# Performance work log

Measured on AMD Instinct MI355X. Metric: run time of the kernel, lower is better.

The kernel has to match this reference:

```python
import jax, jax.numpy as jnp
import numpy as np

EMB = 768
HEADS = 12
HEAD_DIM = EMB // HEADS


def setup_inputs() -> dict:
    key = jax.random.key(0)
    ks = jax.random.split(key, 9)
    B, L, D = 4, 2048, EMB
    s = 1.0 / np.sqrt(D)
    return {
        "x": jax.random.normal(ks[0], (B, L, D), dtype=jnp.float32),
        "Wq": jax.random.normal(ks[1], (D, D), dtype=jnp.float32) * s,
        "bq": jnp.zeros((D,), dtype=jnp.float32),
        "Wk": jax.random.normal(ks[2], (D, D), dtype=jnp.float32) * s,
        "bk": jnp.zeros((D,), dtype=jnp.float32),
        "Wv": jax.random.normal(ks[3], (D, D), dtype=jnp.float32) * s,
        "bv": jnp.zeros((D,), dtype=jnp.float32),
        "Wo": jax.random.normal(ks[4], (D, D), dtype=jnp.float32) * s,
        "bo": jnp.zeros((D,), dtype=jnp.float32),
    }


def reference(x, Wq, bq, Wk, bk, Wv, bv, Wo, bo):
    B, L, D = x.shape
    H, hd = HEADS, HEAD_DIM
    # QKV projections -> [B, H, L, hd]
    def proj(W, b):
        return (x @ W + b).reshape(B, L, H, hd).transpose(0, 2, 1, 3)
    Q = proj(Wq, bq)
    K = proj(Wk, bk)
    V = proj(Wv, bv)
    # scores [B, H, L, L]
    scores = jnp.einsum("bhqd,bhkd->bhqk", Q, K) / jnp.sqrt(jnp.float32(hd))
    attn = jax.nn.softmax(scores, axis=-1)
    out = jnp.einsum("bhqk,bhkd->bhqd", attn, V)  # [B,H,L,hd]
    out = out.transpose(0, 2, 1, 3).reshape(B, L, D)
    return out @ Wo + bo
```

## Files before the change

### kernel.cpp

```cpp
#include <hip/hip_runtime.h>
#include <math.h>

#define TL 2048
#define TD 768
#define NH 12
#define HD 64
#define NB 4
#define MTOT (NB * TL)

typedef __bf16 bf16;
typedef __attribute__((ext_vector_type(4))) __bf16 bf16x4;
typedef __attribute__((ext_vector_type(8))) __bf16 bf16x8;
typedef __attribute__((ext_vector_type(4))) float floatx4;

#define QSCALE 0.18033688011112042f

#define MFMA16(A, B, C) __builtin_amdgcn_mfma_f32_16x16x32_bf16(A, B, C, 0, 0, 0)

__device__ __forceinline__ void gl_lds16(const void* g, void* l) {
    __builtin_amdgcn_global_load_lds(
        (const __attribute__((address_space(1))) void*)g,
        (__attribute__((address_space(3))) void*)l, 16, 0, 0);
}

__device__ __forceinline__ floatx4 exp2x4(floatx4 a) {
    floatx4 r;
    r.x = __builtin_amdgcn_exp2f(a.x);
    r.y = __builtin_amdgcn_exp2f(a.y);
    r.z = __builtin_amdgcn_exp2f(a.z);
    r.w = __builtin_amdgcn_exp2f(a.w);
    return r;
}

__device__ __forceinline__ int kperm_inv(int r) {
    return (r & 35) | (((r >> 2) & 3) << 3) | (((r >> 4) & 1) << 2);
}

__global__ __launch_bounds__(256)
void prep_kernel(const float* __restrict__ x, bf16* __restrict__ xb,
                 const float* __restrict__ W0, const float* __restrict__ W1,
                 const float* __restrict__ W2, const float* __restrict__ W3,
                 bf16* __restrict__ T0, bf16* __restrict__ T1,
                 bf16* __restrict__ T2, bf16* __restrict__ T3)
{
    __shared__ float Ts[64][65];
    const int t = threadIdx.x;

    if (blockIdx.x < 6144) {
        size_t i = ((size_t)blockIdx.x * 256 + t) * 4;
        float4 v = *(const float4*)(x + i);
        bf16x4 o;
        o[0] = (bf16)v.x; o[1] = (bf16)v.y; o[2] = (bf16)v.z; o[3] = (bf16)v.w;
        *(bf16x4*)(xb + i) = o;
        return;
    }

    const int bid = blockIdx.x - 6144;
    const int z = bid / 144, rem = bid % 144;
    const float* W = z == 0 ? W0 : z == 1 ? W1 : z == 2 ? W2 : W3;
    bf16*       T = z == 0 ? T0 : z == 1 ? T1 : z == 2 ? T2 : T3;
    const int k0 = (rem % 12) * 64, n0 = (rem / 12) * 64;
    const int rr = t >> 4, cc = (t & 15) * 4;
#pragma unroll
    for (int i = 0; i < 4; ++i) {
        int row = rr + i * 16;
        float4 v = *(const float4*)(W + (size_t)(k0 + row) * TD + n0 + cc);
        Ts[row][cc] = v.x; Ts[row][cc + 1] = v.y;
        Ts[row][cc + 2] = v.z; Ts[row][cc + 3] = v.w;
    }
    __syncthreads();
#pragma unroll
    for (int i = 0; i < 4; ++i) {
        int n = rr + i * 16;
        bf16x4 pk;
#pragma unroll
        for (int j = 0; j < 4; ++j) pk[j] = (bf16)Ts[cc + j][n];
        *(bf16x4*)(T + (size_t)(n0 + n) * TD + k0 + cc) = pk;
    }
}

__global__ __launch_bounds__(256)
void qkv_gemm(const bf16* __restrict__ xb,
              const bf16* __restrict__ Wqt, const bf16* __restrict__ Wkt,
              const bf16* __restrict__ Wvt,
              const float* __restrict__ bq, const float* __restrict__ bk,
              const float* __restrict__ bv,
              bf16* __restrict__ Q, bf16* __restrict__ K, bf16* __restrict__ Vt)
{
    __shared__ __align__(16) bf16 SM[2 * 128 * 64];
    bf16* As = SM;
    bf16* Bs = SM + 128 * 64;

    const int t = threadIdx.x;
    const int lane = t & 63, w = t >> 6;
    const int quad = lane >> 4, l16 = lane & 15;
    const int m0 = blockIdx.x * 128;
    const int n0 = blockIdx.y * 128;
    const int which = blockIdx.z;
    const bf16*  W    = which == 0 ? Wqt : which == 1 ? Wkt : Wvt;
    const float* bias = which == 0 ? bq  : which == 1 ? bk  : bv;
    const float scale = which == 0 ? QSCALE : 1.0f;

    const int rm = (w >> 1) * 64, cn = (w & 1) * 64;

    floatx4 acc[4][4];
#pragma unroll
    for (int i = 0; i < 4; ++i)
#pragma unroll
        for (int j = 0; j < 4; ++j) acc[i][j] = (floatx4){0.f, 0.f, 0.f, 0.f};

    const bf16* gA[4];
    const bf16* gB[4];
#pragma unroll
    for (int i = 0; i < 4; ++i) {
        int n = t + i * 256, r = n >> 3, s = ((n & 7) ^ (r & 7)) * 8;
        gA[i] = xb + (size_t)(m0 + r) * TD + s;
        gB[i] = W + (size_t)(n0 + r) * TD + s;
    }

    for (int kk = 0; kk < TD; kk += 64) {
#pragma unroll
        for (int i = 0; i < 4; ++i) {
            gl_lds16(gA[i] + kk, As + t * 8 + i * 2048);
            gl_lds16(gB[i] + kk, Bs + t * 8 + i * 2048);
        }
        __syncthreads();
#pragma unroll
        for (int ks = 0; ks < 2; ++ks) {
            bf16x8 af[4], bfr[4];
#pragma unroll
            for (int mb = 0; mb < 4; ++mb) {
                int r = rm + mb * 16 + l16;
                af[mb] = *(const bf16x8*)&As[r * 64 + (((ks * 4 + quad) ^ (r & 7)) * 8)];
            }
#pragma unroll
            for (int nb = 0; nb < 4; ++nb) {
                int r = cn + nb * 16 + l16;
                bfr[nb] = *(const bf16x8*)&Bs[r * 64 + (((ks * 4 + quad) ^ (r & 7)) * 8)];
            }
#pragma unroll
            for (int mb = 0; mb < 4; ++mb)
#pragma unroll
                for (int nb = 0; nb < 4; ++nb)
                    acc[mb][nb] = MFMA16(af[mb], bfr[nb], acc[mb][nb]);
        }
        __syncthreads();
    }

    float bsc[4];
#pragma unroll
    for (int nb = 0; nb < 4; ++nb)
        bsc[nb] = bias[n0 + cn + nb * 16 + l16] * scale;

    const int token0 = m0 + rm;
    const int b  = token0 >> 11;
    const int l0 = token0 & (TL - 1);
    const int h  = (n0 + cn) >> 6;
    const int bh = b * NH + h;
    bf16* Ew = SM + w * (16 * 72);

    if (which < 2) {
        bf16* gp = (which == 0 ? Q : K) + ((size_t)bh * TL + l0) * HD;
#pragma unroll
        for (int mb = 0; mb < 4; ++mb) {
#pragma unroll
            for (int nb = 0; nb < 4; ++nb)
#pragma unroll
                for (int r = 0; r < 4; ++r)
                    Ew[(quad * 4 + r) * 72 + nb * 16 + l16] =
                        (bf16)(acc[mb][nb][r] * scale + bsc[nb]);
#pragma unroll
            for (int i = 0; i < 2; ++i) {
                int row = i * 8 + (lane >> 3), seg = lane & 7;
                bf16x8 v = *(const bf16x8*)&Ew[row * 72 + seg * 8];
                *(bf16x8*)(gp + (size_t)(mb * 16 + row) * HD + seg * 8) = v;
            }
        }
    } else {
#pragma unroll
        for (int nb = 0; nb < 4; ++nb) {
#pragma unroll
            for (int mb = 0; mb < 4; ++mb) {
                bf16x4 pk;
#pragma unroll
                for (int r = 0; r < 4; ++r) pk[r] = (bf16)(acc[mb][nb][r] + bsc[nb]);
                *(bf16x4*)&Ew[l16 * 72 + mb * 16 + quad * 4] = pk;
            }
#pragma unroll
            for (int i = 0; i < 2; ++i) {
                int row = i * 8 + (lane >> 3), seg = lane & 7;
                bf16x8 v = *(const bf16x8*)&Ew[row * 72 + seg * 8];
                *(bf16x8*)(Vt + ((size_t)bh * HD + nb * 16 + row) * TL + l0 + seg * 8) = v;
            }
        }
    }
}

__global__ __launch_bounds__(256)
void attn_kernel(const bf16* __restrict__ Q, const bf16* __restrict__ K,
                 const bf16* __restrict__ Vt, bf16* __restrict__ O)
{
    __shared__ __align__(16) bf16 Ks[64 * 64];
    __shared__ __align__(16) bf16 Vs[64 * 64];

    const int t = threadIdx.x;
    const int lane = t & 63, w = t >> 6;
    const int quad = lane >> 4, l16 = lane & 15;

    const int n = blockIdx.y * gridDim.x + blockIdx.x;
    const int xcd = n & 7, s = n >> 3;
    const int bh = xcd * 6 + (s >> 4);
    const int q0 = (s & 15) * 128;

    const bf16* Qb = Q + (size_t)bh * TL * HD;
    const bf16* Kb = K + (size_t)bh * TL * HD;
    const bf16* Vb = Vt + (size_t)bh * HD * TL;

    const int qw = q0 + w * 32;
    bf16x8 qf[2][2];
#pragma unroll
    for (int mb = 0; mb < 2; ++mb)
#pragma unroll
        for (int ks = 0; ks < 2; ++ks)
            qf[mb][ks] = *(const bf16x8*)(Qb + (size_t)(qw + mb * 16 + l16) * HD
                                          + ks * 32 + quad * 8);

    float lrow[2] = {0.f, 0.f};
    floatx4 o[2][4];
#pragma unroll
    for (int mb = 0; mb < 2; ++mb)
#pragma unroll
        for (int db = 0; db < 4; ++db) o[mb][db] = (floatx4){0.f, 0.f, 0.f, 0.f};

    const bf16* gK[2];
    const bf16* gV[2];
#pragma unroll
    for (int i = 0; i < 2; ++i) {
        int nn = t + i * 256, r = nn >> 3, sg = ((nn & 7) ^ (r & 7)) * 8;
        gK[i] = Kb + (size_t)kperm_inv(r) * HD + sg;
        gV[i] = Vb + (size_t)r * TL + sg;
    }

    for (int kt = 0; kt < TL / 64; ++kt) {
        const int k0 = kt * 64;
        __syncthreads();
#pragma unroll
        for (int i = 0; i < 2; ++i) {
            gl_lds16(gK[i] + (size_t)k0 * HD, Ks + t * 8 + i * 2048);
            gl_lds16(gV[i] + k0,              Vs + t * 8 + i * 2048);
        }
        __syncthreads();

        floatx4 s2[2][4];
#pragma unroll
        for (int nb = 0; nb < 4; ++nb) {
            int r = nb * 16 + l16;
            bf16x8 kf0 = *(const bf16x8*)&Ks[r * 64 + ((quad ^ (r & 7)) * 8)];
            bf16x8 kf1 = *(const bf16x8*)&Ks[r * 64 + (((4 + quad) ^ (r & 7)) * 8)];
#pragma unroll
            for (int mb = 0; mb < 2; ++mb) {
                floatx4 a = (floatx4){0.f, 0.f, 0.f, 0.f};
                a = MFMA16(kf0, qf[mb][0], a);
                a = MFMA16(kf1, qf[mb][1], a);
                s2[mb][nb] = a;
            }
        }

        bf16x8 pA[2][2];
#pragma unroll
        for (int mb = 0; mb < 2; ++mb) {
#pragma unroll
            for (int ks = 0; ks < 2; ++ks) {
                floatx4 p0 = exp2x4(s2[mb][2 * ks]);
                floatx4 p1 = exp2x4(s2[mb][2 * ks + 1]);
                lrow[mb] += (p0.x + p0.y + p0.z + p0.w) + (p1.x + p1.y + p1.z + p1.w);
                bf16x8 pk;
                pk[0] = (bf16)p0.x; pk[1] = (bf16)p0.y; pk[2] = (bf16)p0.z; pk[3] = (bf16)p0.w;
                pk[4] = (bf16)p1.x; pk[5] = (bf16)p1.y; pk[6] = (bf16)p1.z; pk[7] = (bf16)p1.w;
                pA[mb][ks] = pk;
            }
        }

#pragma unroll
        for (int ks = 0; ks < 2; ++ks) {
#pragma unroll
            for (int db = 0; db < 4; ++db) {
                int r = db * 16 + l16;
                bf16x8 vf = *(const bf16x8*)&Vs[r * 64 + (((ks * 4 + quad) ^ (r & 7)) * 8)];
#pragma unroll
                for (int mb = 0; mb < 2; ++mb)
                    o[mb][db] = MFMA16(pA[mb][ks], vf, o[mb][db]);
            }
        }
    }

    const int b = bh / NH, h = bh % NH;
#pragma unroll
    for (int mb = 0; mb < 2; ++mb) {
        lrow[mb] += __shfl_xor(lrow[mb], 16);
        lrow[mb] += __shfl_xor(lrow[mb], 32);
        floatx4 inv;
#pragma unroll
        for (int r = 0; r < 4; ++r)
            inv[r] = 1.0f / __shfl(lrow[mb], (lane & 48) | (quad * 4 + r));
#pragma unroll
        for (int db = 0; db < 4; ++db)
#pragma unroll
            for (int r = 0; r < 4; ++r) {
                int l = qw + mb * 16 + quad * 4 + r;
                O[((size_t)b * TL + l) * TD + h * HD + db * 16 + l16] =
                    (bf16)(o[mb][db][r] * inv[r]);
            }
    }
}

__global__ __launch_bounds__(256)
void oproj_gemm(const bf16* __restrict__ A, const bf16* __restrict__ Wt,
                const float* __restrict__ bo, float* __restrict__ out)
{
    __shared__ __align__(16) bf16 SM[2 * 128 * 64];
    bf16* As = SM;
    bf16* Bs = SM + 128 * 64;

    const int t = threadIdx.x;
    const int lane = t & 63, w = t >> 6;
    const int quad = lane >> 4, l16 = lane & 15;
    const int m0 = blockIdx.x * 128;
    const int n0 = blockIdx.y * 128;
    const int rm = (w >> 1) * 64, cn = (w & 1) * 64;

    floatx4 acc[4][4];
#pragma unroll
    for (int i = 0; i < 4; ++i)
#pragma unroll
        for (int j = 0; j < 4; ++j) acc[i][j] = (floatx4){0.f, 0.f, 0.f, 0.f};

    const bf16* gA[4];
    const bf16* gB[4];
#pragma unroll
    for (int i = 0; i < 4; ++i) {
        int n = t + i * 256, r = n >> 3, s = ((n & 7) ^ (r & 7)) * 8;
        gA[i] = A + (size_t)(m0 + r) * TD + s;
        gB[i] = Wt + (size_t)(n0 + r) * TD + s;
    }

    for (int kk = 0; kk < TD; kk += 64) {
#pragma unroll
        for (int i = 0; i < 4; ++i) {
            gl_lds16(gA[i] + kk, As + t * 8 + i * 2048);
            gl_lds16(gB[i] + kk, Bs + t * 8 + i * 2048);
        }
        __syncthreads();
#pragma unroll
        for (int ks = 0; ks < 2; ++ks) {
            bf16x8 af[4], bfr[4];
#pragma unroll
            for (int mb = 0; mb < 4; ++mb) {
                int r = rm + mb * 16 + l16;
                af[mb] = *(const bf16x8*)&As[r * 64 + (((ks * 4 + quad) ^ (r & 7)) * 8)];
            }
#pragma unroll
            for (int nb = 0; nb < 4; ++nb) {
                int r = cn + nb * 16 + l16;
                bfr[nb] = *(const bf16x8*)&Bs[r * 64 + (((ks * 4 + quad) ^ (r & 7)) * 8)];
            }
#pragma unroll
            for (int mb = 0; mb < 4; ++mb)
#pragma unroll
                for (int nb = 0; nb < 4; ++nb)
                    acc[mb][nb] = MFMA16(af[mb], bfr[nb], acc[mb][nb]);
        }
        __syncthreads();
    }

    float bb[4];
#pragma unroll
    for (int nb = 0; nb < 4; ++nb) bb[nb] = bo[n0 + cn + nb * 16 + l16];

    float* Ew = (float*)SM + w * (16 * 68);
#pragma unroll
    for (int mb = 0; mb < 4; ++mb) {
#pragma unroll
        for (int nb = 0; nb < 4; ++nb)
#pragma unroll
            for (int r = 0; r < 4; ++r)
                Ew[(quad * 4 + r) * 68 + nb * 16 + l16] = acc[mb][nb][r] + bb[nb];
#pragma unroll
        for (int i = 0; i < 4; ++i) {
            int row = i * 4 + (lane >> 4), seg = lane & 15;
            float4 v = *(const float4*)&Ew[row * 68 + seg * 4];
            *(float4*)(out + (size_t)(m0 + rm + mb * 16 + row) * TD + n0 + cn + seg * 4) = v;
        }
    }
}

extern "C" void kernel_launch(void* const* d_in, const int* in_sizes, int n_in,
                              void* d_out, int out_size, void* d_ws, size_t ws_size,
                              hipStream_t stream)
{
    const float* x  = (const float*)d_in[0];
    const float* Wq = (const float*)d_in[1];
    const float* bq = (const float*)d_in[2];
    const float* Wk = (const float*)d_in[3];
    const float* bk = (const float*)d_in[4];
    const float* Wv = (const float*)d_in[5];
    const float* bv = (const float*)d_in[6];
    const float* Wo = (const float*)d_in[7];
    const float* bo = (const float*)d_in[8];

    const size_t NXE = (size_t)MTOT * TD;
    const size_t NWE = (size_t)TD * TD;

    bf16* xb  = (bf16*)d_ws;
    bf16* Wqt = xb + NXE;
    bf16* Wkt = Wqt + NWE;
    bf16* Wvt = Wkt + NWE;
    bf16* Wot = Wvt + NWE;
    bf16* Qb  = Wot + NWE;
    bf16* Kb  = Qb + NXE;
    bf16* Vtb = Kb + NXE;
    bf16* Ob  = Vtb + NXE;

    prep_kernel<<<6144 + 576, 256, 0, stream>>>(x, xb, Wq, Wk, Wv, Wo,
                                                Wqt, Wkt, Wvt, Wot);
    qkv_gemm<<<dim3(MTOT / 128, TD / 128, 3), 256, 0, stream>>>(
        xb, Wqt, Wkt, Wvt, bq, bk, bv, Qb, Kb, Vtb);
    attn_kernel<<<dim3(TL / 128, NB * NH), 256, 0, stream>>>(Qb, Kb, Vtb, Ob);
    oproj_gemm<<<dim3(MTOT / 128, TD / 128), 256, 0, stream>>>(Ob, Wot, bo,
                                                               (float*)d_out);
}
```

Baseline: 217.8 us.

## Fuse all four stages into one cooperative persistent kernel with grid syncs

Adds a cooperative mega-kernel of 768 blocks that runs prep, QKV GEMM, attention and output projection in sequence, separated by grid.sync, replacing four separate launches. The GEMM tiles are rewritten with a K-step of 32 and smaller shared memory, so three blocks fit per CU. The aim is to remove launch gaps and tail effects between kernels. In exchange, occupancy is capped by the cooperative launch, phases can idle at grid barriers, and the QKV phase runs 1152 tiles over 768 blocks in two uneven rounds. It falls back to the old four-kernel path if a cooperative launch is not possible.

Result: no change. 216.0 us (-0.8%).

```diff
diff --git a/kernel.cpp b/kernel.cpp
--- a/kernel.cpp
+++ b/kernel.cpp
@@ -1,5 +1,8 @@
 #include <hip/hip_runtime.h>
+#include <hip/hip_cooperative_groups.h>
 #include <math.h>
+
+namespace cg = cooperative_groups;
 
 #define TL 2048
 #define TD 768
@@ -34,6 +37,390 @@
 
 __device__ __forceinline__ int kperm_inv(int r) {
     return (r & 35) | (((r >> 2) & 3) << 3) | (((r >> 4) & 1) << 2);
+}
+
+
+__device__ __forceinline__ void attn_phase(
+    char* smem, int n,
+    const bf16* __restrict__ Q, const bf16* __restrict__ K,
+    const bf16* __restrict__ Vt, bf16* __restrict__ O)
+{
+    bf16* Ks = (bf16*)smem;
+    bf16* Vs = Ks + 64 * 64;
+
+    const int t = threadIdx.x;
+    const int lane = t & 63, w = t >> 6;
+    const int quad = lane >> 4, l16 = lane & 15;
+
+    const int xcd = n & 7, s = n >> 3;
+    const int bh = xcd * 6 + (s >> 4);
+    const int q0 = (s & 15) * 128;
+
+    const bf16* Qb = Q + (size_t)bh * TL * HD;
+    const bf16* Kb = K + (size_t)bh * TL * HD;
+    const bf16* Vb = Vt + (size_t)bh * HD * TL;
+
+    const int qw = q0 + w * 32;
+    bf16x8 qf[2][2];
+#pragma unroll
+    for (int mb = 0; mb < 2; ++mb)
+#pragma unroll
+        for (int ks = 0; ks < 2; ++ks)
+            qf[mb][ks] = *(const bf16x8*)(Qb + (size_t)(qw + mb * 16 + l16) * HD
+                                          + ks * 32 + quad * 8);
+
+    float lrow[2] = {0.f, 0.f};
+    floatx4 o[2][4];
+#pragma unroll
+    for (int mb = 0; mb < 2; ++mb)
+#pragma unroll
+        for (int db = 0; db < 4; ++db) o[mb][db] = (floatx4){0.f, 0.f, 0.f, 0.f};
+
+    const bf16* gK[2];
+    const bf16* gV[2];
+#pragma unroll
+    for (int i = 0; i < 2; ++i) {
+        int nn = t + i * 256, r = nn >> 3, sg = ((nn & 7) ^ (r & 7)) * 8;
+        gK[i] = Kb + (size_t)kperm_inv(r) * HD + sg;
+        gV[i] = Vb + (size_t)r * TL + sg;
+    }
+
+    for (int kt = 0; kt < TL / 64; ++kt) {
+        const int k0 = kt * 64;
+        __syncthreads();
+#pragma unroll
+        for (int i = 0; i < 2; ++i) {
+            gl_lds16(gK[i] + (size_t)k0 * HD, Ks + t * 8 + i * 2048);
+            gl_lds16(gV[i] + k0,              Vs + t * 8 + i * 2048);
+        }
+        __syncthreads();
+
+        floatx4 s2[2][4];
+#pragma unroll
+        for (int nb = 0; nb < 4; ++nb) {
+            int r = nb * 16 + l16;
+            bf16x8 kf0 = *(const bf16x8*)&Ks[r * 64 + ((quad ^ (r & 7)) * 8)];
+            bf16x8 kf1 = *(const bf16x8*)&Ks[r * 64 + (((4 + quad) ^ (r & 7)) * 8)];
+#pragma unroll
+            for (int mb = 0; mb < 2; ++mb) {
+                floatx4 a = (floatx4){0.f, 0.f, 0.f, 0.f};
+                a = MFMA16(kf0, qf[mb][0], a);
+                a = MFMA16(kf1, qf[mb][1], a);
+                s2[mb][nb] = a;
+            }
+        }
+
+        bf16x8 pA[2][2];
+#pragma unroll
+        for (int mb = 0; mb < 2; ++mb) {
+#pragma unroll
+            for (int ks = 0; ks < 2; ++ks) {
+                floatx4 p0 = exp2x4(s2[mb][2 * ks]);
+                floatx4 p1 = exp2x4(s2[mb][2 * ks + 1]);
+                lrow[mb] += (p0.x + p0.y + p0.z + p0.w) + (p1.x + p1.y + p1.z + p1.w);
+                bf16x8 pk;
+                pk[0] = (bf16)p0.x; pk[1] = (bf16)p0.y; pk[2] = (bf16)p0.z; pk[3] = (bf16)p0.w;
+                pk[4] = (bf16)p1.x; pk[5] = (bf16)p1.y; pk[6] = (bf16)p1.z; pk[7] = (bf16)p1.w;
+                pA[mb][ks] = pk;
+            }
+        }
+
+#pragma unroll
+        for (int ks = 0; ks < 2; ++ks) {
+#pragma unroll
+            for (int db = 0; db < 4; ++db) {
+                int r = db * 16 + l16;
+                bf16x8 vf = *(const bf16x8*)&Vs[r * 64 + (((ks * 4 + quad) ^ (r & 7)) * 8)];
+#pragma unroll
+                for (int mb = 0; mb < 2; ++mb)
+                    o[mb][db] = MFMA16(pA[mb][ks], vf, o[mb][db]);
+            }
+        }
+    }
+
+    const int b = bh / NH, h = bh % NH;
+#pragma unroll
+    for (int mb = 0; mb < 2; ++mb) {
+        lrow[mb] += __shfl_xor(lrow[mb], 16);
+        lrow[mb] += __shfl_xor(lrow[mb], 32);
+        floatx4 inv;
+#pragma unroll
+        for (int r = 0; r < 4; ++r)
+            inv[r] = 1.0f / __shfl(lrow[mb], (lane & 48) | (quad * 4 + r));
+#pragma unroll
+        for (int db = 0; db < 4; ++db)
+#pragma unroll
+            for (int r = 0; r < 4; ++r) {
+                int l = qw + mb * 16 + quad * 4 + r;
+                O[((size_t)b * TL + l) * TD + h * HD + db * 16 + l16] =
+                    (bf16)(o[mb][db][r] * inv[r]);
+            }
+    }
+}
+
+__device__ __forceinline__ void qkv_tile32(
+    char* smem, int m0, int n0, int which,
+    const bf16* __restrict__ xb,
+    const bf16* __restrict__ Wqt, const bf16* __restrict__ Wkt,
+    const bf16* __restrict__ Wvt,
+    const float* __restrict__ bq, const float* __restrict__ bk,
+    const float* __restrict__ bv,
+    bf16* __restrict__ Q, bf16* __restrict__ K, bf16* __restrict__ Vt)
+{
+    bf16* As = (bf16*)smem;
+    bf16* Bs = As + 128 * 32;
+
+    const int t = threadIdx.x;
+    const int lane = t & 63, w = t >> 6;
+    const int quad = lane >> 4, l16 = lane & 15;
+    const bf16*  W    = which == 0 ? Wqt : which == 1 ? Wkt : Wvt;
+    const float* bias = which == 0 ? bq  : which == 1 ? bk  : bv;
+    const float scale = which == 0 ? QSCALE : 1.0f;
+    const int rm = (w >> 1) * 64, cn = (w & 1) * 64;
+
+    floatx4 acc[4][4];
+#pragma unroll
+    for (int i = 0; i < 4; ++i)
+#pragma unroll
+        for (int j = 0; j < 4; ++j) acc[i][j] = (floatx4){0.f, 0.f, 0.f, 0.f};
+
+    const bf16* gA[2];
+    const bf16* gB[2];
+#pragma unroll
+    for (int i = 0; i < 2; ++i) {
+        int nn = t + i * 256, r = nn >> 2;
+        int sg = (((nn & 3) ^ ((r ^ (r >> 2)) & 3))) * 8;
+        gA[i] = xb + (size_t)(m0 + r) * TD + sg;
+        gB[i] = W + (size_t)(n0 + r) * TD + sg;
+    }
+
+    __syncthreads();
+
+    for (int kk = 0; kk < TD; kk += 32) {
+#pragma unroll
+        for (int i = 0; i < 2; ++i) {
+            gl_lds16(gA[i] + kk, As + t * 8 + i * 2048);
+            gl_lds16(gB[i] + kk, Bs + t * 8 + i * 2048);
+        }
+        __syncthreads();
+        bf16x8 af[4], bfr[4];
+#pragma unroll
+        for (int mb = 0; mb < 4; ++mb) {
+            int r = rm + mb * 16 + l16;
+            af[mb] = *(const bf16x8*)&As[r * 32 + ((quad ^ ((r ^ (r >> 2)) & 3)) * 8)];
+        }
+#pragma unroll
+        for (int nb = 0; nb < 4; ++nb) {
+            int r = cn + nb * 16 + l16;
+            bfr[nb] = *(const bf16x8*)&Bs[r * 32 + ((quad ^ ((r ^ (r >> 2)) & 3)) * 8)];
+        }
+#pragma unroll
+        for (int mb = 0; mb < 4; ++mb)
+#pragma unroll
+            for (int nb = 0; nb < 4; ++nb)
+                acc[mb][nb] = MFMA16(af[mb], bfr[nb], acc[mb][nb]);
+        __syncthreads();
+    }
+
+    float bsc[4];
+#pragma unroll
+    for (int nb = 0; nb < 4; ++nb)
+        bsc[nb] = bias[n0 + cn + nb * 16 + l16] * scale;
+
+    const int token0 = m0 + rm;
+    const int b  = token0 >> 11;
+    const int l0 = token0 & (TL - 1);
+    const int h  = (n0 + cn) >> 6;
+    const int bh = b * NH + h;
+    bf16* Ew = (bf16*)smem + w * (16 * 72);
+
+    if (which < 2) {
+        bf16* gp = (which == 0 ? Q : K) + ((size_t)bh * TL + l0) * HD;
+#pragma unroll
+        for (int mb = 0; mb < 4; ++mb) {
+#pragma unroll
+            for (int nb = 0; nb < 4; ++nb)
+#pragma unroll
+                for (int r = 0; r < 4; ++r)
+                    Ew[(quad * 4 + r) * 72 + nb * 16 + l16] =
+                        (bf16)(acc[mb][nb][r] * scale + bsc[nb]);
+#pragma unroll
+            for (int i = 0; i < 2; ++i) {
+                int row = i * 8 + (lane >> 3), seg = lane & 7;
+                bf16x8 v = *(const bf16x8*)&Ew[row * 72 + seg * 8];
+                *(bf16x8*)(gp + (size_t)(mb * 16 + row) * HD + seg * 8) = v;
+            }
+        }
+    } else {
+#pragma unroll
+        for (int nb = 0; nb < 4; ++nb) {
+#pragma unroll
+            for (int mb = 0; mb < 4; ++mb) {
+                bf16x4 pk;
+#pragma unroll
+                for (int r = 0; r < 4; ++r) pk[r] = (bf16)(acc[mb][nb][r] + bsc[nb]);
+                *(bf16x4*)&Ew[l16 * 72 + mb * 16 + quad * 4] = pk;
+            }
+#pragma unroll
+            for (int i = 0; i < 2; ++i) {
+                int row = i * 8 + (lane >> 3), seg = lane & 7;
+                bf16x8 v = *(const bf16x8*)&Ew[row * 72 + seg * 8];
+                *(bf16x8*)(Vt + ((size_t)bh * HD + nb * 16 + row) * TL + l0 + seg * 8) = v;
+            }
+        }
+    }
+}
+
+__device__ __forceinline__ void oproj_tile32(
+    char* smem, int m0, int n0,
+    const bf16* __restrict__ A, const bf16* __restrict__ Wt,
+    const float* __restrict__ bo, float* __restrict__ out)
+{
+    bf16* As = (bf16*)smem;
+    bf16* Bs = As + 128 * 32;
+
+    const int t = threadIdx.x;
+    const int lane = t & 63, w = t >> 6;
+    const int quad = lane >> 4, l16 = lane & 15;
+    const int rm = (w >> 1) * 64, cn = (w & 1) * 64;
+
+    floatx4 acc[4][4];
+#pragma unroll
+    for (int i = 0; i < 4; ++i)
+#pragma unroll
+        for (int j = 0; j < 4; ++j) acc[i][j] = (floatx4){0.f, 0.f, 0.f, 0.f};
+
+    const bf16* gA[2];
+    const bf16* gB[2];
+#pragma unroll
+    for (int i = 0; i < 2; ++i) {
+        int nn = t + i * 256, r = nn >> 2;
+        int sg = (((nn & 3) ^ ((r ^ (r >> 2)) & 3))) * 8;
+        gA[i] = A + (size_t)(m0 + r) * TD + sg;
+        gB[i] = Wt + (size_t)(n0 + r) * TD + sg;
+    }
+
+    for (int kk = 0; kk < TD; kk += 32) {
+#pragma unroll
+        for (int i = 0; i < 2; ++i) {
+            gl_lds16(gA[i] + kk, As + t * 8 + i * 2048);
+            gl_lds16(gB[i] + kk, Bs + t * 8 + i * 2048);
+        }
+        __syncthreads();
+        bf16x8 af[4], bfr[4];
+#pragma unroll
+        for (int mb = 0; mb < 4; ++mb) {
+            int r = rm + mb * 16 + l16;
+            af[mb] = *(const bf16x8*)&As[r * 32 + ((quad ^ ((r ^ (r >> 2)) & 3)) * 8)];
+        }
+#pragma unroll
+        for (int nb = 0; nb < 4; ++nb) {
+            int r = cn + nb * 16 + l16;
+            bfr[nb] = *(const bf16x8*)&Bs[r * 32 + ((quad ^ ((r ^ (r >> 2)) & 3)) * 8)];
+        }
+#pragma unroll
+        for (int mb = 0; mb < 4; ++mb)
+#pragma unroll
+            for (int nb = 0; nb < 4; ++nb)
+                acc[mb][nb] = MFMA16(af[mb], bfr[nb], acc[mb][nb]);
+        __syncthreads();
+    }
+
+    float bb[4];
+#pragma unroll
+    for (int nb = 0; nb < 4; ++nb) bb[nb] = bo[n0 + cn + nb * 16 + l16];
+
+    float* Ew = (float*)smem + w * (16 * 68);
+#pragma unroll
+    for (int mb = 0; mb < 4; ++mb) {
+#pragma unroll
+        for (int nb = 0; nb < 4; ++nb)
+#pragma unroll
+            for (int r = 0; r < 4; ++r)
+                Ew[(quad * 4 + r) * 68 + nb * 16 + l16] = acc[mb][nb][r] + bb[nb];
+#pragma unroll
+        for (int i = 0; i < 4; ++i) {
+            int row = i * 4 + (lane >> 4), seg = lane & 15;
+            float4 v = *(const float4*)&Ew[row * 68 + seg * 4];
+            *(float4*)(out + (size_t)(m0 + rm + mb * 16 + row) * TD + n0 + cn + seg * 4) = v;
+        }
+    }
+}
+
+__global__ __launch_bounds__(256, 3)
+void mega_kernel(const float* __restrict__ x,
+                 const float* __restrict__ Wq, const float* __restrict__ bq,
+                 const float* __restrict__ Wk, const float* __restrict__ bk,
+                 const float* __restrict__ Wv, const float* __restrict__ bv,
+                 const float* __restrict__ Wo, const float* __restrict__ bo,
+                 bf16* xb, bf16* Wqt, bf16* Wkt, bf16* Wvt, bf16* Wot,
+                 bf16* Qb, bf16* Kb, bf16* Vtb, bf16* Ob,
+                 float* out)
+{
+    __shared__ __align__(16) char smem[21504];
+    const int t = threadIdx.x;
+    const int bid = blockIdx.x;
+    cg::grid_group grid = cg::this_grid();
+
+    {
+        size_t base = (size_t)bid * 8192 + t * 4;
+#pragma unroll
+        for (int p = 0; p < 8; ++p) {
+            float4 v = *(const float4*)(x + base + p * 1024);
+            bf16x4 o4;
+            o4[0] = (bf16)v.x; o4[1] = (bf16)v.y;
+            o4[2] = (bf16)v.z; o4[3] = (bf16)v.w;
+            *(bf16x4*)(xb + base + p * 1024) = o4;
+        }
+        if (bid < 576) {
+            const int z = bid / 144, rem = bid % 144;
+            const float* W = z == 0 ? Wq : z == 1 ? Wk : z == 2 ? Wv : Wo;
+            bf16*       T = z == 0 ? Wqt : z == 1 ? Wkt : z == 2 ? Wvt : Wot;
+            const int k0 = (rem % 12) * 64, n0 = (rem / 12) * 64;
+            float* Ts = (float*)smem;
+            const int rr = t >> 4, cc = (t & 15) * 4;
+#pragma unroll
+            for (int i = 0; i < 4; ++i) {
+                int row = rr + i * 16;
+                float4 v = *(const float4*)(W + (size_t)(k0 + row) * TD + n0 + cc);
+                Ts[row * 65 + cc]     = v.x; Ts[row * 65 + cc + 1] = v.y;
+                Ts[row * 65 + cc + 2] = v.z; Ts[row * 65 + cc + 3] = v.w;
+            }
+            __syncthreads();
+#pragma unroll
+            for (int i = 0; i < 4; ++i) {
+                int n = rr + i * 16;
+                bf16x4 pk;
+#pragma unroll
+                for (int j = 0; j < 4; ++j) pk[j] = (bf16)Ts[(cc + j) * 65 + n];
+                *(bf16x4*)(T + (size_t)(n0 + n) * TD + k0 + cc) = pk;
+            }
+        }
+    }
+    __threadfence();
+    grid.sync();
+    __threadfence();
+
+#pragma unroll 1
+    for (int p = 0; p < 2; ++p) {
+        int tt = bid + p * 768;
+        if (tt < 1152) {
+            int which = tt / 384, r = tt % 384;
+            qkv_tile32(smem, (r & 63) * 128, (r >> 6) * 128, which,
+                       xb, Wqt, Wkt, Wvt, bq, bk, bv, Qb, Kb, Vtb);
+        }
+    }
+    __threadfence();
+    grid.sync();
+    __threadfence();
+
+    attn_phase(smem, bid, Qb, Kb, Vtb, Ob);
+    __threadfence();
+    grid.sync();
+    __threadfence();
+
+    if (bid < 384)
+        oproj_tile32(smem, (bid & 63) * 128, (bid >> 6) * 128, Ob, Wot, bo, out);
 }
 
 __global__ __launch_bounds__(256)
@@ -100,7 +487,6 @@
     const bf16*  W    = which == 0 ? Wqt : which == 1 ? Wkt : Wvt;
     const float* bias = which == 0 ? bq  : which == 1 ? bk  : bv;
     const float scale = which == 0 ? QSCALE : 1.0f;
-
     const int rm = (w >> 1) * 64, cn = (w & 1) * 64;
 
     floatx4 acc[4][4];
@@ -200,118 +586,9 @@
 void attn_kernel(const bf16* __restrict__ Q, const bf16* __restrict__ K,
                  const bf16* __restrict__ Vt, bf16* __restrict__ O)
 {
-    __shared__ __align__(16) bf16 Ks[64 * 64];
-    __shared__ __align__(16) bf16 Vs[64 * 64];
-
-    const int t = threadIdx.x;
-    const int lane = t & 63, w = t >> 6;
-    const int quad = lane >> 4, l16 = lane & 15;
-
+    __shared__ __align__(16) char smem[16384];
     const int n = blockIdx.y * gridDim.x + blockIdx.x;
-    const int xcd = n & 7, s = n >> 3;
-    const int bh = xcd * 6 + (s >> 4);
-    const int q0 = (s & 15) * 128;
-
-    const bf16* Qb = Q + (size_t)bh * TL * HD;
-    const bf16* Kb = K + (size_t)bh * TL * HD;
-    const bf16* Vb = Vt + (size_t)bh * HD * TL;
-
-    const int qw = q0 + w * 32;
-    bf16x8 qf[2][2];
-#pragma unroll
-    for (int mb = 0; mb < 2; ++mb)
-#pragma unroll
-        for (int ks = 0; ks < 2; ++ks)
-            qf[mb][ks] = *(const bf16x8*)(Qb + (size_t)(qw + mb * 16 + l16) * HD
-                                          + ks * 32 + quad * 8);
-
-    float lrow[2] = {0.f, 0.f};
-    floatx4 o[2][4];
-#pragma unroll
-    for (int mb = 0; mb < 2; ++mb)
-#pragma unroll
-        for (int db = 0; db < 4; ++db) o[mb][db] = (floatx4){0.f, 0.f, 0.f, 0.f};
-
-    const bf16* gK[2];
-    const bf16* gV[2];
-#pragma unroll
-    for (int i = 0; i < 2; ++i) {
-        int nn = t + i * 256, r = nn >> 3, sg = ((nn & 7) ^ (r & 7)) * 8;
-        gK[i] = Kb + (size_t)kperm_inv(r) * HD + sg;
-        gV[i] = Vb + (size_t)r * TL + sg;
-    }
-
-    for (int kt = 0; kt < TL / 64; ++kt) {
-        const int k0 = kt * 64;
-        __syncthreads();
-#pragma unroll
-        for (int i = 0; i < 2; ++i) {
-            gl_lds16(gK[i] + (size_t)k0 * HD, Ks + t * 8 + i * 2048);
-            gl_lds16(gV[i] + k0,              Vs + t * 8 + i * 2048);
-        }
-        __syncthreads();
-
-        floatx4 s2[2][4];
-#pragma unroll
-        for (int nb = 0; nb < 4; ++nb) {
-            int r = nb * 16 + l16;
-            bf16x8 kf0 = *(const bf16x8*)&Ks[r * 64 + ((quad ^ (r & 7)) * 8)];
-            bf16x8 kf1 = *(const bf16x8*)&Ks[r * 64 + (((4 + quad) ^ (r & 7)) * 8)];
-#pragma unroll
-            for (int mb = 0; mb < 2; ++mb) {
-                floatx4 a = (floatx4){0.f, 0.f, 0.f, 0.f};
-                a = MFMA16(kf0, qf[mb][0], a);
-                a = MFMA16(kf1, qf[mb][1], a);
-                s2[mb][nb] = a;
-            }
-        }
-
-        bf16x8 pA[2][2];
-#pragma unroll
-        for (int mb = 0; mb < 2; ++mb) {
-#pragma unroll
-            for (int ks = 0; ks < 2; ++ks) {
-                floatx4 p0 = exp2x4(s2[mb][2 * ks]);
-                floatx4 p1 = exp2x4(s2[mb][2 * ks + 1]);
-                lrow[mb] += (p0.x + p0.y + p0.z + p0.w) + (p1.x + p1.y + p1.z + p1.w);
-                bf16x8 pk;
-                pk[0] = (bf16)p0.x; pk[1] = (bf16)p0.y; pk[2] = (bf16)p0.z; pk[3] = (bf16)p0.w;
-                pk[4] = (bf16)p1.x; pk[5] = (bf16)p1.y; pk[6] = (bf16)p1.z; pk[7] = (bf16)p1.w;
-                pA[mb][ks] = pk;
-            }
-        }
-
-#pragma unroll
-        for (int ks = 0; ks < 2; ++ks) {
-#pragma unroll
-            for (int db = 0; db < 4; ++db) {
-                int r = db * 16 + l16;
-                bf16x8 vf = *(const bf16x8*)&Vs[r * 64 + (((ks * 4 + quad) ^ (r & 7)) * 8)];
-#pragma unroll
-                for (int mb = 0; mb < 2; ++mb)
-                    o[mb][db] = MFMA16(pA[mb][ks], vf, o[mb][db]);
-            }
-        }
-    }
-
-    const int b = bh / NH, h = bh % NH;
-#pragma unroll
-    for (int mb = 0; mb < 2; ++mb) {
-        lrow[mb] += __shfl_xor(lrow[mb], 16);
-        lrow[mb] += __shfl_xor(lrow[mb], 32);
-        floatx4 inv;
-#pragma unroll
-        for (int r = 0; r < 4; ++r)
-            inv[r] = 1.0f / __shfl(lrow[mb], (lane & 48) | (quad * 4 + r));
-#pragma unroll
-        for (int db = 0; db < 4; ++db)
-#pragma unroll
-            for (int r = 0; r < 4; ++r) {
-                int l = qw + mb * 16 + quad * 4 + r;
-                O[((size_t)b * TL + l) * TD + h * HD + db * 16 + l16] =
-                    (bf16)(o[mb][db][r] * inv[r]);
-            }
-    }
+    attn_phase(smem, n, Q, K, Vt, O);
 }
 
 __global__ __launch_bounds__(256)
@@ -420,6 +697,32 @@
     bf16* Kb  = Qb + NXE;
     bf16* Vtb = Kb + NXE;
     bf16* Ob  = Vtb + NXE;
+    float* outp = (float*)d_out;
+
+    static int use_coop = -1;
+    if (use_coop < 0) {
+        int coop = 0, ncu = 0, nb = 0;
+        hipDeviceGetAttribute(&coop, hipDeviceAttributeCooperativeLaunch, 0);
+        hipDeviceGetAttribute(&ncu, hipDeviceAttributeMultiprocessorCount, 0);
+        hipOccupancyMaxActiveBlocksPerMultiprocessor(&nb, mega_kernel, 256, 0);
+        use_coop = (coop && (long)nb * ncu >= 768) ? 1 : 0;
+    }
+
+    if (use_coop) {
+        void* args[] = {
+            (void*)&x,
+            (void*)&Wq, (void*)&bq, (void*)&Wk, (void*)&bk,
+            (void*)&Wv, (void*)&bv, (void*)&Wo, (void*)&bo,
+            (void*)&xb, (void*)&Wqt, (void*)&Wkt, (void*)&Wvt, (void*)&Wot,
+            (void*)&Qb, (void*)&Kb, (void*)&Vtb, (void*)&Ob,
+            (void*)&outp
+        };
+        hipError_t e = hipLaunchCooperativeKernel((const void*)mega_kernel,
+                                                  dim3(768), dim3(256), args,
+                                                  0, stream);
+        if (e == hipSuccess) return;
+        use_coop = 0;
+    }
 
     prep_kernel<<<6144 + 576, 256, 0, stream>>>(x, xb, Wq, Wk, Wv, Wo,
                                                 Wqt, Wkt, Wvt, Wot);
```
